# Performance work log

Measured on AMD Instinct MI355X. Metric: run time of the kernel, lower is better.

Reference implementation:

```python
import jax, jax.numpy as jnp
import numpy as np

B, N, D, H, DH = 64, 512, 128, 4, 32  # graphs, nodes/graph, emb_dim, heads, head_dim
E = 8192  # edges per graph (avg degree 16)


def setup_inputs() -> dict:
    key = jax.random.key(0)
    ks = jax.random.split(key, 12)
    total_nodes = B * N
    # within-graph random edges, then shift to global node ids
    src = jax.random.randint(ks[0], (B, E), 0, N)
    dst = jax.random.randint(ks[1], (B, E), 0, N)
    offs = (jnp.arange(B) * N)[:, None]
    edge_index = jnp.stack([(src + offs).reshape(-1), (dst + offs).reshape(-1)], axis=0)
    batch = jnp.repeat(jnp.arange(B), N)
    inner = H * DH
    s = lambda d: 1.0 / np.sqrt(d)
    return {
        "x": jax.random.normal(ks[2], (total_nodes, D), jnp.float32),
        "edge_index": edge_index,
        "edge_embedding": jax.random.normal(ks[3], (B * E, D), jnp.float32),
        "batch": batch,
        "W_gcn": jax.random.normal(ks[4], (D, D), jnp.float32) * s(D),
        "b_gcn": jnp.zeros((D,), jnp.float32),
        "root_emb": jax.random.normal(ks[5], (1, D), jnp.float32),
        "Wq": jax.random.normal(ks[6], (D, inner), jnp.float32) * s(D),
        "Wkv": jax.random.normal(ks[7], (D, 2 * inner), jnp.float32) * s(D),
        "Wout": jax.random.normal(ks[8], (inner, D), jnp.float32) * s(inner),
        "b_out": jnp.zeros((D,), jnp.float32),
    }


def reference(x, edge_index, edge_embedding, batch, W_gcn, b_gcn, root_emb, Wq, Wkv, Wout, b_out):
    total_nodes = x.shape[0]
    row, col = edge_index[0], edge_index[1]
    # ---- GCNConv ----
    h = x @ W_gcn + b_gcn
    deg = jax.ops.segment_sum(jnp.ones_like(row, dtype=h.dtype), row, num_segments=total_nodes) + 1.0
    dinv = deg ** -0.5  # deg >= 1, no inf
    norm = dinv[row] * dinv[col]
    msg = norm[:, None] * jax.nn.relu(h[row] + edge_embedding)
    agg = jax.ops.segment_sum(msg, col, num_segments=total_nodes)
    h = agg + jax.nn.relu(h + root_emb) / deg[:, None]
    # ---- dense batch (uniform graph sizes -> reshape) + masked self-attention ----
    nf = h.reshape(B, N, D)
    q = (nf @ Wq).reshape(B, N, H, DH)
    kv = nf @ Wkv
    k = kv[..., : H * DH].reshape(B, N, H, DH)
    v = kv[..., H * DH :].reshape(B, N, H, DH)
    scale = DH ** -0.5
    sim = jnp.einsum("bihd,bjhd->bhij", q, k) * scale
    attn = jax.nn.softmax(sim, axis=-1)  # all-true node mask (uniform batches)
    out = jnp.einsum("bhij,bjhd->bihd", attn, v).reshape(B, N, H * DH)
    out = out @ Wout + b_out
    return out.reshape(total_nodes, D)
```

## Files before the change

### kernel.cpp

```cpp
#include <hip/hip_runtime.h>
#include <hip/hip_bf16.h>

#define TOTAL_NODES 32768
#define NNODE 512
#define ETOT 524288

typedef unsigned short u16;
typedef __attribute__((ext_vector_type(8))) short bf16x8;
typedef __attribute__((ext_vector_type(4))) float f32x4;

union U8 { bf16x8 v; u16 s[8]; uint4 q; };

__device__ __forceinline__ float bf2f(u16 u) {
    union { unsigned int i; float f; } x; x.i = ((unsigned int)u) << 16; return x.f;
}
__device__ __forceinline__ u16 f2bf(float f) {
    union { __hip_bfloat16 h; u16 u; } c; c.h = __float2bfloat16(f); return c.u;
}
__device__ __forceinline__ f32x4 mfma16(bf16x8 a, bf16x8 b, f32x4 c) {
    return __builtin_amdgcn_mfma_f32_16x16x32_bf16(a, b, c, 0, 0, 0);
}

__global__ void hist_kernel(const int* __restrict__ ei, int* __restrict__ cnt_row,
                            int* __restrict__ cnt_col) {
    int e = blockIdx.x * blockDim.x + threadIdx.x;
    if (e < ETOT) {
        atomicAdd(&cnt_row[ei[e]], 1);
        atomicAdd(&cnt_col[ei[ETOT + e]], 1);
    }
}

__global__ __launch_bounds__(1024) void scan_kernel(const int* __restrict__ cnt,
                                                    int* __restrict__ offs,
                                                    int* __restrict__ cur,
                                                    const int* __restrict__ cnt_row,
                                                    float* __restrict__ dinv) {
    __shared__ int part[1024];
    const int t = threadIdx.x;
    const int base = t * 32;
    int local[32];
    int s = 0;
#pragma unroll
    for (int i = 0; i < 32; i++) { local[i] = s; s += cnt[base + i]; }
    part[t] = s;
    __syncthreads();
    for (int off = 1; off < 1024; off <<= 1) {
        int v = (t >= off) ? part[t - off] : 0;
        __syncthreads();
        part[t] += v;
        __syncthreads();
    }
    int prefix = (t == 0) ? 0 : part[t - 1];
#pragma unroll
    for (int i = 0; i < 32; i++) {
        int o = prefix + local[i];
        offs[base + i] = o;
        cur[base + i] = o;
    }
    if (t == 1023) offs[32768] = prefix + s;
#pragma unroll
    for (int i = 0; i < 32; i++)
        dinv[base + i] = rsqrtf((float)cnt_row[base + i] + 1.0f);
}

__global__ void scatter_kernel(const int* __restrict__ ei, int* __restrict__ cur,
                               int2* __restrict__ pairs) {
    int e = blockIdx.x * blockDim.x + threadIdx.x;
    if (e < ETOT) {
        int r = ei[e], c = ei[ETOT + e];
        int pos = atomicAdd(&cur[c], 1);
        pairs[pos] = make_int2(r, e);
    }
}

__global__ __launch_bounds__(128) void gather_kernel(const int2* __restrict__ pairs,
                                                     const int* __restrict__ offs,
                                                     const int* __restrict__ cnt_row,
                                                     const float* __restrict__ dinv,
                                                     const float* __restrict__ h0,
                                                     const float* __restrict__ ee,
                                                     const float* __restrict__ root,
                                                     float* __restrict__ h) {
    const int c = blockIdx.x;
    const int d = threadIdx.x;
    const int s = offs[c], e_end = offs[c + 1];
    float acc = 0.0f;
    int i = s;
    for (; i + 2 <= e_end; i += 2) {
        int2 p0 = pairs[i], p1 = pairs[i + 1];
        float d0 = dinv[p0.x], d1 = dinv[p1.x];
        float v0 = h0[(size_t)p0.x * 128 + d] + ee[(size_t)p0.y * 128 + d];
        float v1 = h0[(size_t)p1.x * 128 + d] + ee[(size_t)p1.y * 128 + d];
        acc += fmaxf(v0, 0.0f) * d0 + fmaxf(v1, 0.0f) * d1;
    }
    for (; i < e_end; i++) {
        int2 p0 = pairs[i];
        float v0 = h0[(size_t)p0.x * 128 + d] + ee[(size_t)p0.y * 128 + d];
        acc += fmaxf(v0, 0.0f) * dinv[p0.x];
    }
    float degc = (float)cnt_row[c] + 1.0f;
    float hv = h0[(size_t)c * 128 + d] + root[d];
    h[(size_t)c * 128 + d] = dinv[c] * acc + fmaxf(hv, 0.0f) / degc;
}

__global__ __launch_bounds__(256) void wprep_kernel(const float* __restrict__ Wg,
                                                    const float* __restrict__ Wq,
                                                    const float* __restrict__ Wkv,
                                                    const float* __restrict__ Wo,
                                                    u16* __restrict__ wt) {
    int idx = blockIdx.x * 256 + threadIdx.x;
    const float* W; int outc; int local; u16* hi; u16* lo;
    if (idx < 16384)      { W = Wg;  outc = 128; local = idx;         hi = wt;          lo = wt + 16384; }
    else if (idx < 32768) { W = Wq;  outc = 128; local = idx - 16384; hi = wt + 32768;  lo = wt + 49152; }
    else if (idx < 65536) { W = Wkv; outc = 256; local = idx - 32768; hi = wt + 65536;  lo = wt + 98304; }
    else                  { W = Wo;  outc = 128; local = idx - 65536; hi = wt + 131072; lo = wt + 147456; }
    int c = local >> 7, k = local & 127;
    float f = W[(size_t)k * outc + c];
    u16 h = f2bf(f);
    hi[local] = h;
    lo[local] = f2bf(f - bf2f(h));
}

__global__ __launch_bounds__(256) void mgemm_kernel(const float* __restrict__ in,
                                                    const u16* __restrict__ wthi,
                                                    const u16* __restrict__ wtlo,
                                                    const float* __restrict__ bias,
                                                    float* __restrict__ outp) {
    __shared__ __align__(16) u16 ahi[64 * 136];
    __shared__ __align__(16) u16 alo[64 * 136];
    const int t = threadIdx.x;
    const int rb = blockIdx.x * 64;
    for (int i = t; i < 8192; i += 256) {
        int r = i >> 7, k = i & 127;
        float f = in[(size_t)(rb + r) * 128 + k];
        u16 h = f2bf(f);
        ahi[r * 136 + k] = h;
        alo[r * 136 + k] = f2bf(f - bf2f(h));
    }
    __syncthreads();
    const int w = t >> 6, L = t & 63, n16 = L & 15, quad = L >> 4;
    const int row0 = w * 16;
    bf16x8 Ah[4], Al[4];
#pragma unroll
    for (int kt = 0; kt < 4; kt++) {
        Ah[kt] = *(const bf16x8*)(ahi + (row0 + n16) * 136 + kt * 32 + quad * 8);
        Al[kt] = *(const bf16x8*)(alo + (row0 + n16) * 136 + kt * 32 + quad * 8);
    }
    const f32x4 zero = {0.f, 0.f, 0.f, 0.f};
#pragma unroll
    for (int ct = 0; ct < 8; ct++) {
        f32x4 acc = zero;
#pragma unroll
        for (int kt = 0; kt < 4; kt++) {
            U8 bh_, bl_;
            bh_.q = *(const uint4*)(wthi + (ct * 16 + n16) * 128 + kt * 32 + quad * 8);
            bl_.q = *(const uint4*)(wtlo + (ct * 16 + n16) * 128 + kt * 32 + quad * 8);
            acc = mfma16(Ah[kt], bh_.v, acc);
            acc = mfma16(Ah[kt], bl_.v, acc);
            acc = mfma16(Al[kt], bh_.v, acc);
        }
        float bv = bias ? bias[ct * 16 + n16] : 0.0f;
#pragma unroll
        for (int r = 0; r < 4; r++)
            outp[(size_t)(rb + row0 + quad * 4 + r) * 128 + ct * 16 + n16] = acc[r] + bv;
    }
}

__global__ __launch_bounds__(256) void qkv_mfma_kernel(const float* __restrict__ in,
                                                       const u16* __restrict__ wt,
                                                       float* __restrict__ qout,
                                                       u16* __restrict__ khi,
                                                       u16* __restrict__ klo,
                                                       u16* __restrict__ vT) {
    __shared__ __align__(16) u16 ahi[64 * 136];
    __shared__ __align__(16) u16 alo[64 * 136];
    const int t = threadIdx.x;
    const int rb = blockIdx.x * 64;
    for (int i = t; i < 8192; i += 256) {
        int r = i >> 7, k = i & 127;
        float f = in[(size_t)(rb + r) * 128 + k];
        u16 h = f2bf(f);
        ahi[r * 136 + k] = h;
        alo[r * 136 + k] = f2bf(f - bf2f(h));
    }
    __syncthreads();
    const int w = t >> 6, L = t & 63, n16 = L & 15, quad = L >> 4;
    const int row0 = w * 16;
    const int b = rb >> 9, rbl = rb & 511;
    bf16x8 Ah[4], Al[4];
#pragma unroll
    for (int kt = 0; kt < 4; kt++) {
        Ah[kt] = *(const bf16x8*)(ahi + (row0 + n16) * 136 + kt * 32 + quad * 8);
        Al[kt] = *(const bf16x8*)(alo + (row0 + n16) * 136 + kt * 32 + quad * 8);
    }
    const f32x4 zero = {0.f, 0.f, 0.f, 0.f};
    const u16* WqT_hi  = wt + 32768;
    const u16* WqT_lo  = wt + 49152;
    const u16* WkvT_hi = wt + 65536;
    const u16* WkvT_lo = wt + 98304;

#pragma unroll
    for (int ct = 0; ct < 8; ct++) {
        f32x4 acc = zero;
#pragma unroll
        for (int kt = 0; kt < 4; kt++) {
            U8 bh_, bl_;
            bh_.q = *(const uint4*)(WqT_hi + (ct * 16 + n16) * 128 + kt * 32 + quad * 8);
            bl_.q = *(const uint4*)(WqT_lo + (ct * 16 + n16) * 128 + kt * 32 + quad * 8);
            acc = mfma16(Ah[kt], bh_.v, acc);
            acc = mfma16(Ah[kt], bl_.v, acc);
            acc = mfma16(Al[kt], bh_.v, acc);
        }
#pragma unroll
        for (int r = 0; r < 4; r++)
            qout[(size_t)(rb + row0 + quad * 4 + r) * 128 + ct * 16 + n16] = acc[r];
    }

#pragma unroll
    for (int ct = 0; ct < 8; ct++) {
        f32x4 acc = zero;
#pragma unroll
        for (int kt = 0; kt < 4; kt++) {
            U8 bh_, bl_;
            bh_.q = *(const uint4*)(WkvT_hi + (ct * 16 + n16) * 128 + kt * 32 + quad * 8);
            bl_.q = *(const uint4*)(WkvT_lo + (ct * 16 + n16) * 128 + kt * 32 + quad * 8);
            acc = mfma16(Ah[kt], bh_.v, acc);
            acc = mfma16(Ah[kt], bl_.v, acc);
            acc = mfma16(Al[kt], bh_.v, acc);
        }
        const int c = ct * 16 + n16, hh = c >> 5, d = c & 31;
        const size_t base = ((size_t)(b * 4 + hh) * 512 + (rbl + row0 + quad * 4)) * 32 + d;
#pragma unroll
        for (int r = 0; r < 4; r++) {
            u16 hv = f2bf(acc[r]);
            khi[base + (size_t)r * 32] = hv;
            klo[base + (size_t)r * 32] = f2bf(acc[r] - bf2f(hv));
        }
    }

#pragma unroll
    for (int ct = 0; ct < 8; ct++) {
        f32x4 acc = zero;
#pragma unroll
        for (int kt = 0; kt < 4; kt++) {
            U8 bh_, bl_;
            bh_.q = *(const uint4*)(WkvT_hi + (128 + ct * 16 + n16) * 128 + kt * 32 + quad * 8);
            bl_.q = *(const uint4*)(WkvT_lo + (128 + ct * 16 + n16) * 128 + kt * 32 + quad * 8);
            acc = mfma16(Ah[kt], bh_.v, acc);
            acc = mfma16(Ah[kt], bl_.v, acc);
            acc = mfma16(Al[kt], bh_.v, acc);
        }
        const int c = ct * 16 + n16, hh = c >> 5, d = c & 31;
        const int n0 = rbl + row0 + quad * 4;
        unsigned int w0 = (unsigned int)f2bf(acc[0]) | ((unsigned int)f2bf(acc[1]) << 16);
        unsigned int w1 = (unsigned int)f2bf(acc[2]) | ((unsigned int)f2bf(acc[3]) << 16);
        uint2 val = make_uint2(w0, w1);
        *(uint2*)(vT + (size_t)(b * 4 + hh) * 16384 + (size_t)(n0 >> 3) * 256 + d * 8 + (n0 & 7)) = val;
    }
}

__global__ __launch_bounds__(256) void attn_mfma_kernel(const float* __restrict__ qbuf,
                                                        const u16* __restrict__ khi,
                                                        const u16* __restrict__ klo,
                                                        const u16* __restrict__ vT,
                                                        float* __restrict__ ao) {
    __shared__ u16 transit[8][16 * 36];
    const int t = threadIdx.x;
    const int w = t >> 6, L = t & 63;
    const int n16 = L & 15, quad = L >> 4;
    const int bh = blockIdx.y, b = bh >> 2, h = bh & 3;
    const int qbase = blockIdx.x * 128 + w * 32;

    bf16x8 qhi[2], qlo[2];
#pragma unroll
    for (int p = 0; p < 2; p++) {
        const float* qp = qbuf + (size_t)(b * 512 + qbase + p * 16 + n16) * 128 + h * 32 + quad * 8;
        U8 uh, ul;
#pragma unroll
        for (int j = 0; j < 8; j++) {
            float f = qp[j] * 0.17677669529663687f;
            u16 hi = f2bf(f);
            uh.s[j] = hi;
            ul.s[j] = f2bf(f - bf2f(hi));
        }
        qhi[p] = uh.v; qlo[p] = ul.v;
    }

    const f32x4 zero = {0.f, 0.f, 0.f, 0.f};

    float m[2][4];
#pragma unroll
    for (int p = 0; p < 2; p++)
#pragma unroll
        for (int r = 0; r < 4; r++) m[p][r] = -1e30f;

    for (int j0 = 0; j0 < 512; j0 += 16) {
        U8 ub; ub.q = *(const uint4*)(khi + (size_t)(bh * 512 + j0 + n16) * 32 + quad * 8);
#pragma unroll
        for (int p = 0; p < 2; p++) {
            f32x4 s = mfma16(qhi[p], ub.v, zero);
#pragma unroll
            for (int r = 0; r < 4; r++) m[p][r] = fmaxf(m[p][r], s[r]);
        }
    }
#pragma unroll
    for (int p = 0; p < 2; p++)
#pragma unroll
        for (int r = 0; r < 4; r++) {
            float mv = m[p][r];
#pragma unroll
            for (int mask = 1; mask < 16; mask <<= 1) mv = fmaxf(mv, __shfl_xor(mv, mask));
            m[p][r] = mv;
        }

    float l[2][4] = {{0.f, 0.f, 0.f, 0.f}, {0.f, 0.f, 0.f, 0.f}};
    f32x4 O[2][2];
#pragma unroll
    for (int p = 0; p < 2; p++)
#pragma unroll
        for (int dt = 0; dt < 2; dt++) O[p][dt] = zero;

    u16* tr[2] = { transit[w * 2 + 0], transit[w * 2 + 1] };

    for (int jb = 0; jb < 512; jb += 32) {
#pragma unroll
        for (int jt = 0; jt < 2; jt++) {
            const int j0 = jb + jt * 16;
            const size_t kidx = (size_t)(bh * 512 + j0 + n16) * 32 + quad * 8;
            U8 uh; uh.q = *(const uint4*)(khi + kidx);
            U8 ul; ul.q = *(const uint4*)(klo + kidx);
#pragma unroll
            for (int p = 0; p < 2; p++) {
                f32x4 s = mfma16(qhi[p], uh.v, zero);
                s = mfma16(qhi[p], ul.v, s);
                s = mfma16(qlo[p], uh.v, s);
#pragma unroll
                for (int r = 0; r < 4; r++) {
                    float pr = __expf(s[r] - m[p][r]);
                    u16 pb = f2bf(pr);
                    l[p][r] += bf2f(pb);
                    tr[p][(quad * 4 + r) * 36 + jt * 16 + n16] = pb;
                }
            }
        }
        bf16x8 A[2];
#pragma unroll
        for (int p = 0; p < 2; p++) {
            const u16* trp = tr[p];
            const int off = n16 * 36 + quad * 8;
            uint2 lo = *(const uint2*)(trp + off);
            uint2 hi2 = *(const uint2*)(trp + off + 4);
            U8 ua; ua.q = make_uint4(lo.x, lo.y, hi2.x, hi2.y);
            A[p] = ua.v;
        }
#pragma unroll
        for (int dt = 0; dt < 2; dt++) {
            U8 uv; uv.q = *(const uint4*)(vT + (size_t)bh * 16384
                                          + (size_t)((jb + quad * 8) >> 3) * 256
                                          + (size_t)(dt * 16 + n16) * 8);
#pragma unroll
            for (int p = 0; p < 2; p++) O[p][dt] = mfma16(A[p], uv.v, O[p][dt]);
        }
    }

#pragma unroll
    for (int p = 0; p < 2; p++)
#pragma unroll
        for (int r = 0; r < 4; r++) {
            float lv = l[p][r];
#pragma unroll
            for (int mask = 1; mask < 16; mask <<= 1) lv += __shfl_xor(lv, mask);
            float inv = 1.0f / lv;
#pragma unroll
            for (int dt = 0; dt < 2; dt++)
                ao[(size_t)(b * 512 + qbase + p * 16 + quad * 4 + r) * 128 + h * 32 + dt * 16 + n16]
                    = O[p][dt][r] * inv;
        }
}

extern "C" void kernel_launch(void* const* d_in, const int* in_sizes, int n_in,
                              void* d_out, int out_size, void* d_ws, size_t ws_size,
                              hipStream_t stream) {
    const float* x    = (const float*)d_in[0];
    const int*   ei   = (const int*)d_in[1];
    const float* ee   = (const float*)d_in[2];
    const float* Wg   = (const float*)d_in[4];
    const float* bg   = (const float*)d_in[5];
    const float* root = (const float*)d_in[6];
    const float* Wq   = (const float*)d_in[7];
    const float* Wkv  = (const float*)d_in[8];
    const float* Wo   = (const float*)d_in[9];
    const float* bo   = (const float*)d_in[10];

    char* ws = (char*)d_ws;
    int*   cnt_row = (int*)ws;
    float* dinv    = (float*)(ws + 131072);
    float* buf1    = (float*)(ws + 262144);
    float* hbuf    = buf1 + 4194304;
    char*  reg3    = (char*)(hbuf + 4194304);
    u16*   khi     = (u16*)reg3;
    u16*   klo     = khi + 4194304;
    u16*   wt      = (u16*)(reg3 + 16777216);
    u16*   vT      = (u16*)d_out;
    int*   cnt_col = (int*)reg3;
    int*   offs    = cnt_col + 32768;
    int*   cur     = offs + 32769;
    int2*  pairs   = (int2*)(cur + 32768 + 1023);

    hipMemsetAsync(cnt_row, 0, 131072, stream);
    hipMemsetAsync(cnt_col, 0, 131072, stream);

    wprep_kernel<<<320, 256, 0, stream>>>(Wg, Wq, Wkv, Wo, wt);

    hist_kernel<<<2048, 256, 0, stream>>>(ei, cnt_row, cnt_col);
    scan_kernel<<<1, 1024, 0, stream>>>(cnt_col, offs, cur, cnt_row, dinv);
    scatter_kernel<<<2048, 256, 0, stream>>>(ei, cur, pairs);

    mgemm_kernel<<<512, 256, 0, stream>>>(x, wt, wt + 16384, bg, buf1);

    gather_kernel<<<32768, 128, 0, stream>>>(pairs, offs, cnt_row, dinv, buf1, ee, root, hbuf);

    qkv_mfma_kernel<<<512, 256, 0, stream>>>(hbuf, wt, buf1, khi, klo, vT);

    attn_mfma_kernel<<<dim3(4, 256), 256, 0, stream>>>(buf1, khi, klo, vT, buf1);

    mgemm_kernel<<<512, 256, 0, stream>>>(buf1, wt + 131072, wt + 147456, bo, (float*)d_out);
}
```

Baseline: 608.6 us.

## Fuse CSR build and weight prep into one per-graph setup kernel

Replaces two memsets and four kernels (weight prep, histogram, single-block scan, scatter) with one setup kernel. Each of 64 blocks builds the CSR for one graph in shared memory, using the fact that edges never leave their graph, while the other 64 blocks convert the weights. This removes launch overhead, global atomics and the serial one-block scan. It relies on edges staying within graph boundaries and on 512 nodes per graph.

```diff
diff --git a/kernel.cpp b/kernel.cpp
--- a/kernel.cpp
+++ b/kernel.cpp
@@ -21,61 +21,75 @@
     return __builtin_amdgcn_mfma_f32_16x16x32_bf16(a, b, c, 0, 0, 0);
 }
 
-__global__ void hist_kernel(const int* __restrict__ ei, int* __restrict__ cnt_row,
-                            int* __restrict__ cnt_col) {
-    int e = blockIdx.x * blockDim.x + threadIdx.x;
-    if (e < ETOT) {
-        atomicAdd(&cnt_row[ei[e]], 1);
-        atomicAdd(&cnt_col[ei[ETOT + e]], 1);
-    }
-}
-
-__global__ __launch_bounds__(1024) void scan_kernel(const int* __restrict__ cnt,
+__global__ __launch_bounds__(512) void setup_kernel(const int* __restrict__ ei,
+                                                    const float* __restrict__ Wg,
+                                                    const float* __restrict__ Wq,
+                                                    const float* __restrict__ Wkv,
+                                                    const float* __restrict__ Wo,
+                                                    u16* __restrict__ wt,
+                                                    float* __restrict__ dinv,
+                                                    float* __restrict__ degf,
                                                     int* __restrict__ offs,
-                                                    int* __restrict__ cur,
-                                                    const int* __restrict__ cnt_row,
-                                                    float* __restrict__ dinv) {
-    __shared__ int part[1024];
+                                                    int2* __restrict__ pairs) {
+    const int blk = blockIdx.x;
     const int t = threadIdx.x;
-    const int base = t * 32;
-    int local[32];
-    int s = 0;
-#pragma unroll
-    for (int i = 0; i < 32; i++) { local[i] = s; s += cnt[base + i]; }
-    part[t] = s;
-    __syncthreads();
-    for (int off = 1; off < 1024; off <<= 1) {
-        int v = (t >= off) ? part[t - off] : 0;
+    if (blk >= 64) {
+        for (int idx = (blk - 64) * 512 + t; idx < 81920; idx += 64 * 512) {
+            const float* W; int outc; int local; u16* hi; u16* lo;
+            if (idx < 16384)      { W = Wg;  outc = 128; local = idx;         hi = wt;          lo = wt + 16384; }
+            else if (idx < 32768) { W = Wq;  outc = 128; local = idx - 16384; hi = wt + 32768;  lo = wt + 49152; }
+            else if (idx < 65536) { W = Wkv; outc = 256; local = idx - 32768; hi = wt + 65536;  lo = wt + 98304; }
+            else                  { W = Wo;  outc = 128; local = idx - 65536; hi = wt + 131072; lo = wt + 147456; }
+            int c = local >> 7, k = local & 127;
+            float f = W[(size_t)k * outc + c];
+            u16 h = f2bf(f);
+            hi[local] = h;
+            lo[local] = f2bf(f - bf2f(h));
+        }
+        return;
+    }
+    __shared__ int cnt_row[512], cnt_col[512], sc[512], cur[512];
+    cnt_row[t] = 0;
+    cnt_col[t] = 0;
+    __syncthreads();
+    const int goff = blk * 8192;
+    int r[16], c[16];
+#pragma unroll
+    for (int i = 0; i < 16; i++) {
+        int e = t + i * 512;
+        r[i] = ei[goff + e];
+        c[i] = ei[ETOT + goff + e];
+        atomicAdd(&cnt_row[r[i] & 511], 1);
+        atomicAdd(&cnt_col[c[i] & 511], 1);
+    }
+    __syncthreads();
+    float dg = (float)cnt_row[t] + 1.0f;
+    degf[blk * 512 + t] = dg;
+    dinv[blk * 512 + t] = rsqrtf(dg);
+    sc[t] = cnt_col[t];
+    __syncthreads();
+    for (int off = 1; off < 512; off <<= 1) {
+        int v = (t >= off) ? sc[t - off] : 0;
         __syncthreads();
-        part[t] += v;
+        sc[t] += v;
         __syncthreads();
     }
-    int prefix = (t == 0) ? 0 : part[t - 1];
-#pragma unroll
-    for (int i = 0; i < 32; i++) {
-        int o = prefix + local[i];
-        offs[base + i] = o;
-        cur[base + i] = o;
-    }
-    if (t == 1023) offs[32768] = prefix + s;
-#pragma unroll
-    for (int i = 0; i < 32; i++)
-        dinv[base + i] = rsqrtf((float)cnt_row[base + i] + 1.0f);
-}
-
-__global__ void scatter_kernel(const int* __restrict__ ei, int* __restrict__ cur,
-                               int2* __restrict__ pairs) {
-    int e = blockIdx.x * blockDim.x + threadIdx.x;
-    if (e < ETOT) {
-        int r = ei[e], c = ei[ETOT + e];
-        int pos = atomicAdd(&cur[c], 1);
-        pairs[pos] = make_int2(r, e);
+    int excl = sc[t] - cnt_col[t];
+    offs[blk * 512 + t] = goff + excl;
+    cur[t] = excl;
+    if (blk == 63 && t == 511) offs[32768] = ETOT;
+    __syncthreads();
+#pragma unroll
+    for (int i = 0; i < 16; i++) {
+        int e = t + i * 512;
+        int pos = atomicAdd(&cur[c[i] & 511], 1);
+        pairs[goff + pos] = make_int2(r[i], goff + e);
     }
 }
 
 __global__ __launch_bounds__(128) void gather_kernel(const int2* __restrict__ pairs,
                                                      const int* __restrict__ offs,
-                                                     const int* __restrict__ cnt_row,
+                                                     const float* __restrict__ degf,
                                                      const float* __restrict__ dinv,
                                                      const float* __restrict__ h0,
                                                      const float* __restrict__ ee,
@@ -98,27 +112,8 @@
         float v0 = h0[(size_t)p0.x * 128 + d] + ee[(size_t)p0.y * 128 + d];
         acc += fmaxf(v0, 0.0f) * dinv[p0.x];
     }
-    float degc = (float)cnt_row[c] + 1.0f;
     float hv = h0[(size_t)c * 128 + d] + root[d];
-    h[(size_t)c * 128 + d] = dinv[c] * acc + fmaxf(hv, 0.0f) / degc;
-}
-
-__global__ __launch_bounds__(256) void wprep_kernel(const float* __restrict__ Wg,
-                                                    const float* __restrict__ Wq,
-                                                    const float* __restrict__ Wkv,
-                                                    const float* __restrict__ Wo,
-                                                    u16* __restrict__ wt) {
-    int idx = blockIdx.x * 256 + threadIdx.x;
-    const float* W; int outc; int local; u16* hi; u16* lo;
-    if (idx < 16384)      { W = Wg;  outc = 128; local = idx;         hi = wt;          lo = wt + 16384; }
-    else if (idx < 32768) { W = Wq;  outc = 128; local = idx - 16384; hi = wt + 32768;  lo = wt + 49152; }
-    else if (idx < 65536) { W = Wkv; outc = 256; local = idx - 32768; hi = wt + 65536;  lo = wt + 98304; }
-    else                  { W = Wo;  outc = 128; local = idx - 65536; hi = wt + 131072; lo = wt + 147456; }
-    int c = local >> 7, k = local & 127;
-    float f = W[(size_t)k * outc + c];
-    u16 h = f2bf(f);
-    hi[local] = h;
-    lo[local] = f2bf(f - bf2f(h));
+    h[(size_t)c * 128 + d] = dinv[c] * acc + fmaxf(hv, 0.0f) / degf[c];
 }
 
 __global__ __launch_bounds__(256) void mgemm_kernel(const float* __restrict__ in,
@@ -393,7 +388,7 @@
     const float* bo   = (const float*)d_in[10];
 
     char* ws = (char*)d_ws;
-    int*   cnt_row = (int*)ws;
+    float* degf    = (float*)ws;
     float* dinv    = (float*)(ws + 131072);
     float* buf1    = (float*)(ws + 262144);
     float* hbuf    = buf1 + 4194304;
@@ -402,23 +397,14 @@
     u16*   klo     = khi + 4194304;
     u16*   wt      = (u16*)(reg3 + 16777216);
     u16*   vT      = (u16*)d_out;
-    int*   cnt_col = (int*)reg3;
-    int*   offs    = cnt_col + 32768;
-    int*   cur     = offs + 32769;
-    int2*  pairs   = (int2*)(cur + 32768 + 1023);
-
-    hipMemsetAsync(cnt_row, 0, 131072, stream);
-    hipMemsetAsync(cnt_col, 0, 131072, stream);
-
-    wprep_kernel<<<320, 256, 0, stream>>>(Wg, Wq, Wkv, Wo, wt);
-
-    hist_kernel<<<2048, 256, 0, stream>>>(ei, cnt_row, cnt_col);
-    scan_kernel<<<1, 1024, 0, stream>>>(cnt_col, offs, cur, cnt_row, dinv);
-    scatter_kernel<<<2048, 256, 0, stream>>>(ei, cur, pairs);
+    int*   offs    = (int*)reg3;
+    int2*  pairs   = (int2*)(reg3 + 262144);
+
+    setup_kernel<<<128, 512, 0, stream>>>(ei, Wg, Wq, Wkv, Wo, wt, dinv, degf, offs, pairs);
 
     mgemm_kernel<<<512, 256, 0, stream>>>(x, wt, wt + 16384, bg, buf1);
 
-    gather_kernel<<<32768, 128, 0, stream>>>(pairs, offs, cnt_row, dinv, buf1, ee, root, hbuf);
+    gather_kernel<<<32768, 128, 0, stream>>>(pairs, offs, degf, dinv, buf1, ee, root, hbuf);
 
     qkv_mfma_kernel<<<512, 256, 0, stream>>>(hbuf, wt, buf1, khi, klo, vT);
 
```

Result: faster. 554.5 us (-8.9%).
